# Kernel tuning notes

Hardware: AMD Instinct MI355X
Metric: run time of the kernel (lower is better)

Reference implementation:

```python
import jax, jax.numpy as jnp
import numpy as np

H = 16
D_MODEL = 1024
D_K = D_MODEL // H
NWORDS = 16384


def setup_inputs() -> dict:
    key0 = jax.random.key(0)
    ks = jax.random.split(key0, 11)
    s = 0.02
    return {
        "query": jax.random.normal(ks[0], (1, D_MODEL), dtype=jnp.float32),
        "key": jax.random.normal(ks[1], (NWORDS, D_MODEL), dtype=jnp.float32),
        "value": jax.random.normal(ks[2], (NWORDS, D_MODEL), dtype=jnp.float32),
        "Wq": jax.random.normal(ks[3], (D_MODEL, D_MODEL), dtype=jnp.float32) * s,
        "bq": jax.random.normal(ks[4], (D_MODEL,), dtype=jnp.float32) * s,
        "Wk": jax.random.normal(ks[5], (D_MODEL, D_MODEL), dtype=jnp.float32) * s,
        "bk": jax.random.normal(ks[6], (D_MODEL,), dtype=jnp.float32) * s,
        "Wv": jax.random.normal(ks[7], (D_MODEL, D_MODEL), dtype=jnp.float32) * s,
        "bv": jax.random.normal(ks[8], (D_MODEL,), dtype=jnp.float32) * s,
        "Wo": jax.random.normal(ks[9], (D_MODEL, D_MODEL), dtype=jnp.float32) * s,
        "bo": jax.random.normal(ks[10], (D_MODEL,), dtype=jnp.float32) * s,
    }


def reference(query, key, value, Wq, bq, Wk, bk, Wv, bv, Wo, bo):
    # torch Linear: y = x @ W.T + b
    q = (query @ Wq.T + bq).reshape(H, D_K)          # [h, d_k]  (single query token)
    k = (key @ Wk.T + bk).reshape(-1, H, D_K)        # [n, h, d_k]
    v = (value @ Wv.T + bv).reshape(-1, H, D_K)      # [n, h, d_k]
    # NOTE: original module applies NO 1/sqrt(d_k) scaling.
    scores = jnp.einsum("hd,nhd->hn", q, k)          # [h, n]
    p_attn = jax.nn.softmax(scores, axis=-1)          # dropout p=0 -> no-op
    x = jnp.einsum("hn,nhd->hd", p_attn, v).reshape(1, H * D_K)  # [1, d_model]
    return x @ Wo.T + bo                              # [1, d_model]
```

## Files before the change

kernel.cpp:

```cpp
#include <hip/hip_runtime.h>

#define DM 1024
#define NW 16384

typedef __attribute__((ext_vector_type(8))) short short8;
typedef __attribute__((ext_vector_type(4))) float f32x4;

#define OFF_AH   1024
#define OFF_AL   9216
#define OFF_D0   17408
#define OFF_S    17424
#define OFF_X    17696
#define OFF_W    18720
#define OFF_E    36864
#define OFF_PART 299008

__device__ __forceinline__ unsigned short f2bf(float f) {
  unsigned int u = __float_as_uint(f);
  return (unsigned short)((u + 0x7fffu + ((u >> 16) & 1u)) >> 16);
}

__global__ __launch_bounds__(256) void k_rowdot(const float* __restrict__ W,
                                                const float* __restrict__ v,
                                                const float* __restrict__ b,
                                                float* __restrict__ out) {
  const int wave = (blockIdx.x * 256 + threadIdx.x) >> 6;
  const int lane = threadIdx.x & 63;
  const float* row = W + (size_t)wave * DM + 4 * lane;
  float s = 0.f;
#pragma unroll
  for (int j = 0; j < 4; ++j) {
    float4 a = *(const float4*)(row + j * 256);
    float4 x = *(const float4*)(v + j * 256 + 4 * lane);
    s += a.x * x.x + a.y * x.y + a.z * x.z + a.w * x.w;
  }
#pragma unroll
  for (int off = 32; off; off >>= 1) s += __shfl_xor(s, off, 64);
  if (lane == 0) out[wave] = s + b[wave];
}

__global__ __launch_bounds__(256) void k_qck(const float* __restrict__ Wq,
                                             const float* __restrict__ bq,
                                             const float* __restrict__ query,
                                             const float* __restrict__ Wk,
                                             const float* __restrict__ bk,
                                             short* __restrict__ Ah,
                                             short* __restrict__ Al,
                                             float* __restrict__ d0,
                                             float* __restrict__ S) {
  const int h = blockIdx.x >> 2;
  const int mc = blockIdx.x & 3;
  const int t = threadIdx.x;
  const int lane = t & 63;
  const int wv = t >> 6;
  __shared__ float qh[64];
  if (blockIdx.x == 0 && t < 16) S[t * 16] = 0.f;
  float4 qv[4];
#pragma unroll
  for (int j = 0; j < 4; ++j) qv[j] = *(const float4*)(query + j * 256 + 4 * lane);
#pragma unroll 1
  for (int i = 0; i < 16; i += 2) {
    const int d0i = 4 * i + wv;
    const int d1i = 4 * (i + 1) + wv;
    const float* r0 = Wq + (size_t)(h * 64 + d0i) * DM + 4 * lane;
    const float* r1 = Wq + (size_t)(h * 64 + d1i) * DM + 4 * lane;
    float4 a0[4], a1[4];
#pragma unroll
    for (int j = 0; j < 4; ++j) { a0[j] = *(const float4*)(r0 + j * 256);
                                  a1[j] = *(const float4*)(r1 + j * 256); }
    float s0 = 0.f, s1 = 0.f;
#pragma unroll
    for (int j = 0; j < 4; ++j) {
      s0 += a0[j].x * qv[j].x + a0[j].y * qv[j].y + a0[j].z * qv[j].z + a0[j].w * qv[j].w;
      s1 += a1[j].x * qv[j].x + a1[j].y * qv[j].y + a1[j].z * qv[j].z + a1[j].w * qv[j].w;
    }
#pragma unroll
    for (int off = 32; off; off >>= 1) { s0 += __shfl_xor(s0, off, 64);
                                         s1 += __shfl_xor(s1, off, 64); }
    if (lane == 0) { qh[d0i] = s0 + bq[h * 64 + d0i];
                     qh[d1i] = s1 + bq[h * 64 + d1i]; }
  }
  __syncthreads();
  const int m = mc * 256 + t;
  const float* Wp = Wk + (size_t)(h * 64) * DM + m;
  float s = 0.f;
#pragma unroll 1
  for (int db = 0; db < 8; ++db) {
    float wv8[8];
#pragma unroll
    for (int j = 0; j < 8; ++j) wv8[j] = Wp[(size_t)(db * 8 + j) * DM];
#pragma unroll
    for (int j = 0; j < 8; ++j) s = fmaf(qh[db * 8 + j], wv8[j], s);
  }
  unsigned short hu = f2bf(s);
  float hf = __uint_as_float(((unsigned int)hu) << 16);
  unsigned short lu = f2bf(s - hf);
  const int kb = m >> 5, q = (m >> 3) & 3, j = m & 7;
  const int idx = (kb * 64 + q * 16 + h) * 8 + j;
  Ah[idx] = (short)hu;
  Al[idx] = (short)lu;
  if (mc == 0 && t == 0) {
    float tt = 0.f;
    for (int d = 0; d < 64; ++d) tt += qh[d] * bk[h * 64 + d];
    d0[h] = tt;
  }
}

__global__ __launch_bounds__(256) void k_scores(const float* __restrict__ key,
                                                const short* __restrict__ AhG,
                                                const short* __restrict__ AlG,
                                                const float* __restrict__ d0,
                                                float* __restrict__ e,
                                                float* __restrict__ S) {
  __shared__ short Ahi[16384];
  __shared__ short Alo[16384];
  const int t = threadIdx.x;
  const int lane = t & 63;
  const int wv = t >> 6;
#pragma unroll
  for (int i = 0; i < 8; ++i) {
    *(short8*)&Ahi[(t + i * 256) * 8] = *(const short8*)&AhG[(t + i * 256) * 8];
    *(short8*)&Alo[(t + i * 256) * 8] = *(const short8*)&AlG[(t + i * 256) * 8];
  }
  __syncthreads();

  const int tile = blockIdx.x * 4 + wv;
  const int n = tile * 16 + (lane & 15);
  const int quad = lane >> 4;
  const float* base = key + (size_t)n * DM + quad * 8;

  f32x4 acc = {0.f, 0.f, 0.f, 0.f};
  float4 f0[4], f1[4];
#pragma unroll
  for (int p = 0; p < 4; ++p) {
    f0[p] = *(const float4*)(base + p * 32);
    f1[p] = *(const float4*)(base + p * 32 + 4);
  }
#pragma unroll
  for (int kb = 0; kb < 32; ++kb) {
    const int slot = kb & 3;
    float4 a0 = f0[slot], a1 = f1[slot];
    if (kb < 28) {
      f0[slot] = *(const float4*)(base + (kb + 4) * 32);
      f1[slot] = *(const float4*)(base + (kb + 4) * 32 + 4);
    }
    short8 ah = *(const short8*)&Ahi[(kb * 64 + lane) * 8];
    short8 al = *(const short8*)&Alo[(kb * 64 + lane) * 8];
    float ff[8] = {a0.x, a0.y, a0.z, a0.w, a1.x, a1.y, a1.z, a1.w};
    short8 bh, bl;
#pragma unroll
    for (int j = 0; j < 8; ++j) {
      unsigned short hu = f2bf(ff[j]);
      bh[j] = (short)hu;
      float hf = __uint_as_float(((unsigned int)hu) << 16);
      bl[j] = (short)f2bf(ff[j] - hf);
    }
    acc = __builtin_amdgcn_mfma_f32_16x16x32_bf16(ah, bh, acc, 0, 0, 0);
    acc = __builtin_amdgcn_mfma_f32_16x16x32_bf16(ah, bl, acc, 0, 0, 0);
    acc = __builtin_amdgcn_mfma_f32_16x16x32_bf16(al, bh, acc, 0, 0, 0);
  }
  const float4 dv = *(const float4*)(d0 + quad * 4);
  float ex0 = __expf(acc[0] + dv.x);
  float ex1 = __expf(acc[1] + dv.y);
  float ex2 = __expf(acc[2] + dv.z);
  float ex3 = __expf(acc[3] + dv.w);
  *(float4*)(e + (size_t)n * 16 + quad * 4) = make_float4(ex0, ex1, ex2, ex3);
  float sr[4] = {ex0, ex1, ex2, ex3};
#pragma unroll
  for (int r = 0; r < 4; ++r) {
    float v = sr[r];
    v += __shfl_xor(v, 1, 64);
    v += __shfl_xor(v, 2, 64);
    v += __shfl_xor(v, 4, 64);
    v += __shfl_xor(v, 8, 64);
    if ((lane & 15) == 0) atomicAdd(S + (size_t)(quad * 4 + r) * 16, v);
  }
}

__global__ __launch_bounds__(256, 2) void k_pv(const float* __restrict__ value,
                                               const float* __restrict__ e,
                                               float* __restrict__ part) {
  const int nb = blockIdx.x >> 2;
  const int mc = blockIdx.x & 3;
  const int t = threadIdx.x;
  const int lane = t & 63;
  const int wy = t >> 6;
  const int col = mc * 256 + lane * 4;
  const int n0 = nb * 256;
  __shared__ float el[256 * 16];
  __shared__ float4 red[2][16][64];
  {
    const float4* eg = (const float4*)(e + (size_t)n0 * 16);
    float4* es = (float4*)el;
#pragma unroll
    for (int k = 0; k < 4; ++k) es[t + k * 256] = eg[t + k * 256];
  }
  __syncthreads();
  float4 acc[16];
#pragma unroll
  for (int h = 0; h < 16; ++h) acc[h] = make_float4(0.f, 0.f, 0.f, 0.f);
  const float* vp = value + (size_t)(n0 + wy * 64) * DM + col;
  const float* ep = &el[wy * 64 * 16];
#pragma unroll 1
  for (int rb = 0; rb < 8; ++rb) {
    float4 v[8];
#pragma unroll
    for (int i = 0; i < 8; ++i) v[i] = *(const float4*)(vp + (size_t)(rb * 8 + i) * DM);
#pragma unroll
    for (int i = 0; i < 8; ++i) {
      const float4* er4 = (const float4*)(ep + (rb * 8 + i) * 16);
      float4 e0 = er4[0], e1 = er4[1], e2 = er4[2], e3 = er4[3];
      float4 vv = v[i];
#define FMA4H(H, P) { acc[H].x = fmaf(P, vv.x, acc[H].x); acc[H].y = fmaf(P, vv.y, acc[H].y); \
                      acc[H].z = fmaf(P, vv.z, acc[H].z); acc[H].w = fmaf(P, vv.w, acc[H].w); }
      FMA4H(0,  e0.x) FMA4H(1,  e0.y) FMA4H(2,  e0.z) FMA4H(3,  e0.w)
      FMA4H(4,  e1.x) FMA4H(5,  e1.y) FMA4H(6,  e1.z) FMA4H(7,  e1.w)
      FMA4H(8,  e2.x) FMA4H(9,  e2.y) FMA4H(10, e2.z) FMA4H(11, e2.w)
      FMA4H(12, e3.x) FMA4H(13, e3.y) FMA4H(14, e3.z) FMA4H(15, e3.w)
#undef FMA4H
    }
  }
  if (wy >= 2) {
#pragma unroll
    for (int h = 0; h < 16; ++h) red[wy - 2][h][lane] = acc[h];
  }
  __syncthreads();
  if (wy < 2) {
#pragma unroll
    for (int h = 0; h < 16; ++h) {
      float4 o = red[wy][h][lane];
      acc[h].x += o.x; acc[h].y += o.y; acc[h].z += o.z; acc[h].w += o.w;
    }
  }
  __syncthreads();
  if (wy == 1) {
#pragma unroll
    for (int h = 0; h < 16; ++h) red[0][h][lane] = acc[h];
  }
  __syncthreads();
  if (wy == 0) {
    float* pp = part + (size_t)nb * (16 * DM) + col;
#pragma unroll
    for (int h = 0; h < 16; ++h) {
      float4 o = red[0][h][lane];
      acc[h].x += o.x; acc[h].y += o.y; acc[h].z += o.z; acc[h].w += o.w;
      *(float4*)(pp + (size_t)h * DM) = acc[h];
    }
  }
}

__global__ __launch_bounds__(256) void k_wred(const float* __restrict__ part,
                                              float* __restrict__ w) {
  const int gid = blockIdx.x * 256 + threadIdx.x;
  const int o = gid >> 2;
  const int q = gid & 3;
  float s = 0.f;
#pragma unroll 1
  for (int ib = 0; ib < 2; ++ib) {
    float x[8];
#pragma unroll
    for (int j = 0; j < 8; ++j) x[j] = part[(size_t)(q * 16 + ib * 8 + j) * 16384 + o];
#pragma unroll
    for (int j = 0; j < 8; ++j) s += x[j];
  }
  s += __shfl_xor(s, 1, 64);
  s += __shfl_xor(s, 2, 64);
  if (q == 0) w[o] = s;
}

__global__ __launch_bounds__(256) void k_xproj(const float* __restrict__ Wv,
                                               const float* __restrict__ w,
                                               const float* __restrict__ bv,
                                               const float* __restrict__ S,
                                               float* __restrict__ x) {
  const int wave = (blockIdx.x * 256 + threadIdx.x) >> 6;
  const int lane = threadIdx.x & 63;
  const int h = wave >> 6;
  const float* vec = w + (size_t)h * DM;
  const float* row = Wv + (size_t)wave * DM + 4 * lane;
  float s = 0.f;
#pragma unroll
  for (int j = 0; j < 4; ++j) {
    float4 a = *(const float4*)(row + j * 256);
    float4 x4 = *(const float4*)(vec + j * 256 + 4 * lane);
    s += a.x * x4.x + a.y * x4.y + a.z * x4.z + a.w * x4.w;
  }
#pragma unroll
  for (int off = 32; off; off >>= 1) s += __shfl_xor(s, off, 64);
  if (lane == 0) x[wave] = s / S[(size_t)h * 16] + bv[wave];
}

extern "C" void kernel_launch(void* const* d_in, const int* in_sizes, int n_in,
                              void* d_out, int out_size, void* d_ws, size_t ws_size,
                              hipStream_t stream) {
  const float* query = (const float*)d_in[0];
  const float* key   = (const float*)d_in[1];
  const float* value = (const float*)d_in[2];
  const float* Wq    = (const float*)d_in[3];
  const float* bq    = (const float*)d_in[4];
  const float* Wk    = (const float*)d_in[5];
  const float* bk    = (const float*)d_in[6];
  const float* Wv    = (const float*)d_in[7];
  const float* bv    = (const float*)d_in[8];
  const float* Wo    = (const float*)d_in[9];
  const float* bo    = (const float*)d_in[10];
  float* out = (float*)d_out;
  float* ws  = (float*)d_ws;
  short* Ah  = (short*)(ws + OFF_AH);
  short* Al  = (short*)(ws + OFF_AL);

  k_qck    <<<64,  256, 0, stream>>>(Wq, bq, query, Wk, bk, Ah, Al, ws + OFF_D0, ws + OFF_S);
  k_scores <<<256, 256, 0, stream>>>(key, Ah, Al, ws + OFF_D0, ws + OFF_E, ws + OFF_S);
  k_pv     <<<256, 256, 0, stream>>>(value, ws + OFF_E, ws + OFF_PART);
  k_wred   <<<256, 256, 0, stream>>>(ws + OFF_PART, ws + OFF_W);
  k_xproj  <<<256, 256, 0, stream>>>(Wv, ws + OFF_W, bv, ws + OFF_S, ws + OFF_X);
  k_rowdot <<<256, 256, 0, stream>>>(Wo, ws + OFF_X, bo, out);
}
```

Measured before the change: 240.8 us.

## Split scores K-dimension across eight waves per tile with LDS reduction

The scores kernel used to give each wave a full 16-row tile and loop over all 32 K-blocks, with the A fragments staged in shared memory. Now each 512-thread block owns one 16-row tile. Each of its 8 waves handles 4 K-blocks, loading A fragments straight from global memory, and the partial accumulators are summed through shared memory before the exp and the atomic row sums. This adds memory-level parallelism and removes the per-block A staging copy. In exchange it costs a block-wide barrier and reduction, and the exp stage runs on one wave per block.

```diff
diff --git a/kernel.cpp b/kernel.cpp
--- a/kernel.cpp
+++ b/kernel.cpp
@@ -106,47 +106,37 @@
   }
 }
 
-__global__ __launch_bounds__(256) void k_scores(const float* __restrict__ key,
+__global__ __launch_bounds__(512) void k_scores(const float* __restrict__ key,
                                                 const short* __restrict__ AhG,
                                                 const short* __restrict__ AlG,
                                                 const float* __restrict__ d0,
                                                 float* __restrict__ e,
                                                 float* __restrict__ S) {
-  __shared__ short Ahi[16384];
-  __shared__ short Alo[16384];
   const int t = threadIdx.x;
   const int lane = t & 63;
   const int wv = t >> 6;
-#pragma unroll
-  for (int i = 0; i < 8; ++i) {
-    *(short8*)&Ahi[(t + i * 256) * 8] = *(const short8*)&AhG[(t + i * 256) * 8];
-    *(short8*)&Alo[(t + i * 256) * 8] = *(const short8*)&AlG[(t + i * 256) * 8];
-  }
-  __syncthreads();
-
-  const int tile = blockIdx.x * 4 + wv;
+  const int tile = blockIdx.x;
   const int n = tile * 16 + (lane & 15);
   const int quad = lane >> 4;
+  const int kb0 = wv * 4;
   const float* base = key + (size_t)n * DM + quad * 8;
-
+  const short8* A8h = (const short8*)AhG;
+  const short8* A8l = (const short8*)AlG;
+
+  short8 ah[4], al[4];
+  float4 f0[4], f1[4];
+#pragma unroll
+  for (int i = 0; i < 4; ++i) {
+    ah[i] = A8h[(kb0 + i) * 64 + lane];
+    al[i] = A8l[(kb0 + i) * 64 + lane];
+    f0[i] = *(const float4*)(base + (kb0 + i) * 32);
+    f1[i] = *(const float4*)(base + (kb0 + i) * 32 + 4);
+  }
   f32x4 acc = {0.f, 0.f, 0.f, 0.f};
-  float4 f0[4], f1[4];
-#pragma unroll
-  for (int p = 0; p < 4; ++p) {
-    f0[p] = *(const float4*)(base + p * 32);
-    f1[p] = *(const float4*)(base + p * 32 + 4);
-  }
-#pragma unroll
-  for (int kb = 0; kb < 32; ++kb) {
-    const int slot = kb & 3;
-    float4 a0 = f0[slot], a1 = f1[slot];
-    if (kb < 28) {
-      f0[slot] = *(const float4*)(base + (kb + 4) * 32);
-      f1[slot] = *(const float4*)(base + (kb + 4) * 32 + 4);
-    }
-    short8 ah = *(const short8*)&Ahi[(kb * 64 + lane) * 8];
-    short8 al = *(const short8*)&Alo[(kb * 64 + lane) * 8];
-    float ff[8] = {a0.x, a0.y, a0.z, a0.w, a1.x, a1.y, a1.z, a1.w};
+#pragma unroll
+  for (int i = 0; i < 4; ++i) {
+    float ff[8] = {f0[i].x, f0[i].y, f0[i].z, f0[i].w,
+                   f1[i].x, f1[i].y, f1[i].z, f1[i].w};
     short8 bh, bl;
 #pragma unroll
     for (int j = 0; j < 8; ++j) {
@@ -155,25 +145,36 @@
       float hf = __uint_as_float(((unsigned int)hu) << 16);
       bl[j] = (short)f2bf(ff[j] - hf);
     }
-    acc = __builtin_amdgcn_mfma_f32_16x16x32_bf16(ah, bh, acc, 0, 0, 0);
-    acc = __builtin_amdgcn_mfma_f32_16x16x32_bf16(ah, bl, acc, 0, 0, 0);
-    acc = __builtin_amdgcn_mfma_f32_16x16x32_bf16(al, bh, acc, 0, 0, 0);
-  }
-  const float4 dv = *(const float4*)(d0 + quad * 4);
-  float ex0 = __expf(acc[0] + dv.x);
-  float ex1 = __expf(acc[1] + dv.y);
-  float ex2 = __expf(acc[2] + dv.z);
-  float ex3 = __expf(acc[3] + dv.w);
-  *(float4*)(e + (size_t)n * 16 + quad * 4) = make_float4(ex0, ex1, ex2, ex3);
-  float sr[4] = {ex0, ex1, ex2, ex3};
-#pragma unroll
-  for (int r = 0; r < 4; ++r) {
-    float v = sr[r];
-    v += __shfl_xor(v, 1, 64);
-    v += __shfl_xor(v, 2, 64);
-    v += __shfl_xor(v, 4, 64);
-    v += __shfl_xor(v, 8, 64);
-    if ((lane & 15) == 0) atomicAdd(S + (size_t)(quad * 4 + r) * 16, v);
+    acc = __builtin_amdgcn_mfma_f32_16x16x32_bf16(ah[i], bh, acc, 0, 0, 0);
+    acc = __builtin_amdgcn_mfma_f32_16x16x32_bf16(ah[i], bl, acc, 0, 0, 0);
+    acc = __builtin_amdgcn_mfma_f32_16x16x32_bf16(al[i], bh, acc, 0, 0, 0);
+  }
+  __shared__ float4 red[8][64];
+  red[wv][lane] = make_float4(acc[0], acc[1], acc[2], acc[3]);
+  __syncthreads();
+  if (wv == 0) {
+    float4 a = red[0][lane];
+#pragma unroll
+    for (int w = 1; w < 8; ++w) {
+      float4 o = red[w][lane];
+      a.x += o.x; a.y += o.y; a.z += o.z; a.w += o.w;
+    }
+    const float4 dv = *(const float4*)(d0 + quad * 4);
+    float ex0 = __expf(a.x + dv.x);
+    float ex1 = __expf(a.y + dv.y);
+    float ex2 = __expf(a.z + dv.z);
+    float ex3 = __expf(a.w + dv.w);
+    *(float4*)(e + (size_t)n * 16 + quad * 4) = make_float4(ex0, ex1, ex2, ex3);
+    float sr[4] = {ex0, ex1, ex2, ex3};
+#pragma unroll
+    for (int r = 0; r < 4; ++r) {
+      float v = sr[r];
+      v += __shfl_xor(v, 1, 64);
+      v += __shfl_xor(v, 2, 64);
+      v += __shfl_xor(v, 4, 64);
+      v += __shfl_xor(v, 8, 64);
+      if ((lane & 15) == 0) atomicAdd(S + (size_t)(quad * 4 + r) * 16, v);
+    }
   }
 }
 
@@ -310,7 +311,7 @@
   short* Al  = (short*)(ws + OFF_AL);
 
   k_qck    <<<64,  256, 0, stream>>>(Wq, bq, query, Wk, bk, Ah, Al, ws + OFF_D0, ws + OFF_S);
-  k_scores <<<256, 256, 0, stream>>>(key, Ah, Al, ws + OFF_D0, ws + OFF_E, ws + OFF_S);
+  k_scores <<<1024,512, 0, stream>>>(key, Ah, Al, ws + OFF_D0, ws + OFF_E, ws + OFF_S);
   k_pv     <<<256, 256, 0, stream>>>(value, ws + OFF_E, ws + OFF_PART);
   k_wred   <<<256, 256, 0, stream>>>(ws + OFF_PART, ws + OFF_W);
   k_xproj  <<<256, 256, 0, stream>>>(Wv, ws + OFF_W, bv, ws + OFF_S, ws + OFF_X);
```

Result: no change. 238.9 us (-0.8%).
